# Kernel tuning notes

Hardware: AMD Instinct MI355X
Metric: run time of the kernel (lower is better)

Reference implementation:

```python
import jax, jax.numpy as jnp
import numpy as np

N_HEADS = 16
HEAD_DIM = 64
LN_EPS = 1e-5


def setup_inputs() -> dict:
    key = jax.random.key(0)
    k1, k2, k3 = jax.random.split(key, 3)
    b, n, d = 4, 2048, 1024
    inner = N_HEADS * HEAD_DIM  # 1024
    x = jax.random.normal(k1, (b, n, d), dtype=jnp.float32)
    ln_gamma = jnp.ones((d,), dtype=jnp.float32)
    ln_beta = jnp.zeros((d,), dtype=jnp.float32)
    # torch Linear weights are [out_features, in_features]
    W_qkv = jax.random.normal(k2, (3 * inner, d), dtype=jnp.float32) * (d ** -0.5)
    W_out = jax.random.normal(k3, (d, inner), dtype=jnp.float32) * (inner ** -0.5)
    return {"x": x, "ln_gamma": ln_gamma, "ln_beta": ln_beta,
            "W_qkv": W_qkv, "W_out": W_out}


def reference(x, ln_gamma, ln_beta, W_qkv, W_out):
    b, n, d = x.shape
    scale = HEAD_DIM ** -0.5
    # LayerNorm over last dim
    mu = jnp.mean(x, axis=-1, keepdims=True)
    var = jnp.mean(jnp.square(x - mu), axis=-1, keepdims=True)
    xn = (x - mu) * jax.lax.rsqrt(var + LN_EPS) * ln_gamma + ln_beta
    # QKV projection (Linear, no bias): y = x @ W^T
    qkv = jnp.einsum('bnd,ed->bne', xn, W_qkv)  # [b, n, 3*inner]
    qkv = qkv.reshape(b, n, 3, N_HEADS, HEAD_DIM)
    q, k, v = (jnp.transpose(qkv[:, :, i], (0, 2, 1, 3)) for i in range(3))  # [b,h,n,hd]
    scores = jnp.einsum('bhqd,bhkd->bhqk', q, k) * scale  # [b,h,n,n]
    attn = jax.nn.softmax(scores, axis=-1)
    out = jnp.einsum('bhqk,bhkd->bhqd', attn, v)  # [b,h,n,hd]
    out = jnp.transpose(out, (0, 2, 1, 3)).reshape(b, n, N_HEADS * HEAD_DIM)
    return jnp.einsum('bni,di->bnd', out, W_out)
```

## Files before the change

### kernel.cpp

```cpp
#include <hip/hip_runtime.h>


typedef _Float16 h16;
typedef __attribute__((ext_vector_type(8))) _Float16 h16x8;
typedef __attribute__((ext_vector_type(4))) _Float16 h16x4;
typedef __attribute__((ext_vector_type(2))) _Float16 h16x2;
typedef __attribute__((ext_vector_type(4))) float f32x4;

#define B_ 4
#define S_ 2048
#define D_ 1024

static __device__ __forceinline__ void async16(void* lds, const void* g) {
  __builtin_amdgcn_global_load_lds((const __attribute__((address_space(1))) void*)g,
                                   (__attribute__((address_space(3))) void*)lds,
                                   16, 0, 0);
}

static __device__ __forceinline__ float ex2(float x) {
  float r;
  asm("v_exp_f32 %0, %1" : "=v"(r) : "v"(x));
  return r;
}

static __device__ __forceinline__ h16x2 pk2(float a, float b) {
  h16x2 r;
  asm("v_cvt_pkrtz_f16_f32 %0, %1, %2" : "=v"(r) : "v"(a), "v"(b));
  return r;
}

union U8 { h16x8 v; h16x2 h[4]; };

__global__ __launch_bounds__(256) void prep_k(const float* __restrict__ x,
                                              const float* __restrict__ g,
                                              const float* __restrict__ be,
                                              h16* __restrict__ xn,
                                              const float* __restrict__ wq,
                                              h16* __restrict__ wqkv,
                                              const float* __restrict__ wo,
                                              h16* __restrict__ wout) {
  const int bid = blockIdx.x;
  const int tid = threadIdx.x;
  if (bid < 8192) {
    const int row = bid;
    const float4 v = ((const float4*)(x + (size_t)row * D_))[tid];
    float s = v.x + v.y + v.z + v.w;
    float s2 = v.x * v.x + v.y * v.y + v.z * v.z + v.w * v.w;
#pragma unroll
    for (int msk = 1; msk < 64; msk <<= 1) {
      s += __shfl_xor(s, msk);
      s2 += __shfl_xor(s2, msk);
    }
    __shared__ float red[8];
    const int wv = tid >> 6, ln = tid & 63;
    if (ln == 0) { red[wv] = s; red[wv + 4] = s2; }
    __syncthreads();
    s = red[0] + red[1] + red[2] + red[3];
    s2 = red[4] + red[5] + red[6] + red[7];
    const float mu = s * (1.f / D_);
    const float rs = rsqrtf(s2 * (1.f / D_) - mu * mu + 1e-5f);
    const float4 gv = ((const float4*)g)[tid];
    const float4 bv = ((const float4*)be)[tid];
    h16x4 o;
    o[0] = (h16)((v.x - mu) * rs * gv.x + bv.x);
    o[1] = (h16)((v.y - mu) * rs * gv.y + bv.y);
    o[2] = (h16)((v.z - mu) * rs * gv.z + bv.z);
    o[3] = (h16)((v.w - mu) * rs * gv.w + bv.w);
    *(h16x4*)(xn + (size_t)row * D_ + tid * 4) = o;
  } else if (bid < 8192 + 3072) {
    const int i = (bid - 8192) * 256 + tid;
    const float4 v = ((const float4*)wq)[i];
    h16x4 r;
    r[0] = (h16)v.x; r[1] = (h16)v.y; r[2] = (h16)v.z; r[3] = (h16)v.w;
    *(h16x4*)(wqkv + (size_t)i * 4) = r;
  } else {
    const int i = (bid - 8192 - 3072) * 256 + tid;
    const float4 v = ((const float4*)wo)[i];
    h16x4 r;
    r[0] = (h16)v.x; r[1] = (h16)v.y; r[2] = (h16)v.z; r[3] = (h16)v.w;
    *(h16x4*)(wout + (size_t)i * 4) = r;
  }
}

__global__ __launch_bounds__(256) void vt_k(const h16* __restrict__ qkv,
                                            h16* __restrict__ vT) {
  __shared__ h16 T[64 * 72];
  const int tid = threadIdx.x;
  const int kv0 = blockIdx.x * 64;
  const int bh = blockIdx.y;
  const int b = bh >> 4, h = bh & 15;
#pragma unroll
  for (int it = 0; it < 2; ++it) {
    const int s = tid + it * 256;
    const int kv = s >> 3, sl = s & 7;
    const int wsl = sl ^ ((kv >> 3) & 7);
    const h16x8 v = *(const h16x8*)(qkv + (size_t)(b * S_ + kv0 + kv) * 3072 + 2048 + h * 64 + sl * 8);
    *(h16x8*)(T + kv * 72 + wsl * 8) = v;
  }
  __syncthreads();
#pragma unroll
  for (int it = 0; it < 2; ++it) {
    const int s = tid + it * 256;
    const int d = s >> 3, sl = s & 7;
    h16x8 v;
#pragma unroll
    for (int j = 0; j < 8; ++j) {
      const int kv = sl * 8 + j;
      v[j] = T[kv * 72 + (((d >> 3) ^ sl) & 7) * 8 + (d & 7)];
    }
    *(h16x8*)(vT + (size_t)(bh * 64 + d) * 2048 + kv0 + sl * 8) = v;
  }
}

template <int BN>
__global__ __launch_bounds__(256, 2) void gemm2(const h16* __restrict__ A, int lda,
                                                const h16* __restrict__ Bm,
                                                float* __restrict__ Cf,
                                                h16* __restrict__ Ch,
                                                int M, int N, int K,
                                                int scale_cols, float scale) {
  constexpr int NB = BN / 32;
  constexpr int JF = BN / 32;
  __shared__ __align__(16) h16 As[2][128 * 64];
  __shared__ __align__(16) h16 Bs[2][BN * 64];
  const int tid = threadIdx.x;
  const int wv = tid >> 6, ln = tid & 63;
  const int l15 = ln & 15, l4 = ln >> 4;
  const int row0 = blockIdx.x * 128, col0 = blockIdx.y * BN;
  const int wm = (wv >> 1) * 64, wn = (wv & 1) * (BN / 2);
  f32x4 acc[4][JF] = {};

  const int srow = wv * 8 + (ln >> 3);
  const int sslot = (ln & 7) ^ ((ln >> 3) & 7);
  const h16* ag = A + (size_t)(row0 + srow) * lda + sslot * 8;
  const h16* bg = Bm + (size_t)(col0 + srow) * K + sslot * 8;

  auto stage = [&](int buf, int t) {
    const size_t k_ = (size_t)t * 64;
#pragma unroll
    for (int c = 0; c < 4; ++c)
      async16((char*)As[buf] + c * 4096 + wv * 1024, ag + (size_t)(c * 32) * lda + k_);
#pragma unroll
    for (int c = 0; c < NB; ++c)
      async16((char*)Bs[buf] + c * 4096 + wv * 1024, bg + (size_t)(c * 32) * K + k_);
  };

  auto compute = [&](int buf) {
    const h16* Ab_ = As[buf];
    const h16* Bb_ = Bs[buf];
#pragma unroll
    for (int ks = 0; ks < 2; ++ks) {
      h16x8 af[4], bf[JF];
#pragma unroll
      for (int i = 0; i < 4; ++i)
        af[i] = *(const h16x8*)(Ab_ + (wm + i * 16 + l15) * 64 +
                                (((ks * 4 + l4) ^ (l15 & 7)) * 8));
#pragma unroll
      for (int j = 0; j < JF; ++j)
        bf[j] = *(const h16x8*)(Bb_ + (wn + j * 16 + l15) * 64 +
                                (((ks * 4 + l4) ^ (l15 & 7)) * 8));
      __builtin_amdgcn_s_setprio(1);
#pragma unroll
      for (int i = 0; i < 4; ++i)
#pragma unroll
        for (int j = 0; j < JF; ++j)
          acc[i][j] = __builtin_amdgcn_mfma_f32_16x16x32_f16(af[i], bf[j], acc[i][j], 0, 0, 0);
      __builtin_amdgcn_s_setprio(0);
    }
  };

  stage(0, 0);
  for (int t = 0; t < 16; ++t) {
    asm volatile("s_waitcnt vmcnt(0) lgkmcnt(0)" ::: "memory");
    __builtin_amdgcn_sched_barrier(0);
    __builtin_amdgcn_s_barrier();
    __builtin_amdgcn_sched_barrier(0);
    if (t + 1 < 16) stage((t + 1) & 1, t + 1);
    compute(t & 1);
  }

#pragma unroll
  for (int i = 0; i < 4; ++i)
#pragma unroll
    for (int j = 0; j < JF; ++j) {
      const int col = col0 + wn + j * 16 + l15;
      const float sc = (col < scale_cols) ? scale : 1.f;
#pragma unroll
      for (int r = 0; r < 4; ++r) {
        const int row = row0 + wm + i * 16 + l4 * 4 + r;
        const float vv = acc[i][j][r] * sc;
        if (Ch) Ch[(size_t)row * N + col] = (h16)vv;
        else    Cf[(size_t)row * N + col] = vv;
      }
    }
}

__global__ __launch_bounds__(512) void attn_k(h16* __restrict__ qkv,
                                              const h16* __restrict__ vT) {
  __shared__ __align__(16) h16 Ks[2][2][64 * 64];
  __shared__ __align__(16) h16 Vs[2][2][64 * 64];
  const int tid = threadIdx.x;
  const int wv = tid >> 6, ln = tid & 63;
  const int l15 = ln & 15, l4 = ln >> 4;
  const int bh = blockIdx.x;
  const int b = bh >> 4, h = bh & 15;
  const size_t rb = (size_t)b * S_;
  const int qb = blockIdx.y * 256 + wv * 32;

  h16x8 qf[2][2];
#pragma unroll
  for (int qb2 = 0; qb2 < 2; ++qb2)
#pragma unroll
    for (int ks = 0; ks < 2; ++ks)
      qf[qb2][ks] = *(const h16x8*)(qkv + (rb + qb + qb2 * 16 + l15) * 3072 + h * 64 + ks * 32 + l4 * 8);

  f32x4 o[2][4] = {};
  f32x4 lsum[2] = {};
  h16x8 ones8;
#pragma unroll
  for (int j = 0; j < 8; ++j) ones8[j] = (h16)1.f;

  const int srow = wv * 8 + (ln >> 3);
  const int ssl = (ln & 7) ^ (srow & 7);
  const h16* kgb = qkv + (rb + srow) * 3072 + 1024 + h * 64 + ssl * 8;

  const int vd = tid >> 3;
  const int s8 = tid & 7;
  const int vks = s8 >> 2, vb0b = s8 & 1, vhi = (s8 >> 1) & 1;
  const int vd7 = vd & 7;
  const h16* vgb = vT + (size_t)(bh * 64 + vd) * 2048 + s8 * 8;
  const int dstA = vd * 64 + (((vks * 4 + (vb0b * 2)) ^ vd7) * 8) + vhi * 4;
  const int dstB = vd * 64 + (((vks * 4 + (vb0b * 2 + 1)) ^ vd7) * 8) + vhi * 4;

  int jro[4], slx[2];
#pragma unroll
  for (int j = 0; j < 4; ++j) jro[j] = (j * 16 + l15) * 64;
#pragma unroll
  for (int ks = 0; ks < 2; ++ks) slx[ks] = ((ks * 4 + l4) ^ (l15 & 7)) * 8;

  h16x8 va0, va1, vb0, vb1;

#define ISSUEK2(BUF, P) do {                                                 \
    const h16* kg_ = kgb + (size_t)(2 * (P)) * 64 * 3072;                    \
    async16((char*)Ks[BUF][0] + wv * 1024, kg_);                             \
    async16((char*)Ks[BUF][1] + wv * 1024, kg_ + (size_t)64 * 3072);         \
  } while (0)

#define VLOAD2(P, R0, R1) do {                                               \
    R0 = *(const h16x8*)(vgb + (2 * (P)) * 64);                              \
    R1 = *(const h16x8*)(vgb + (2 * (P) + 1) * 64);                          \
  } while (0)

#define VSTOREM2(BUF, S0, S1) do {                                           \
    *(h16x4*)(Vs[BUF][0] + dstA) = __builtin_shufflevector(S0, S0, 0, 1, 2, 3); \
    *(h16x4*)(Vs[BUF][0] + dstB) = __builtin_shufflevector(S0, S0, 4, 5, 6, 7); \
    *(h16x4*)(Vs[BUF][1] + dstA) = __builtin_shufflevector(S1, S1, 0, 1, 2, 3); \
    *(h16x4*)(Vs[BUF][1] + dstB) = __builtin_shufflevector(S1, S1, 4, 5, 6, 7); \
  } while (0)

#define COMPUTE1(Kb_, Vb_) do {                                              \
    f32x4 st[2][4] = {};                                                     \
    __builtin_amdgcn_s_setprio(1);                                           \
    _Pragma("unroll")                                                        \
    for (int ks = 0; ks < 2; ++ks) {                                         \
      h16x8 kb[4];                                                           \
      _Pragma("unroll")                                                      \
      for (int jb = 0; jb < 4; ++jb)                                         \
        kb[jb] = *(const h16x8*)(Kb_ + jro[jb] + slx[ks]);                   \
      _Pragma("unroll")                                                      \
      for (int qq = 0; qq < 2; ++qq)                                         \
        _Pragma("unroll")                                                    \
        for (int jb = 0; jb < 4; ++jb)                                       \
          st[qq][jb] = __builtin_amdgcn_mfma_f32_16x16x32_f16(kb[jb], qf[qq][ks], st[qq][jb], 0, 0, 0); \
    }                                                                        \
    __builtin_amdgcn_s_setprio(0);                                           \
    h16x8 vfr[2][4];                                                         \
    _Pragma("unroll")                                                        \
    for (int ks = 0; ks < 2; ++ks)                                           \
      _Pragma("unroll")                                                      \
      for (int jd = 0; jd < 4; ++jd)                                         \
        vfr[ks][jd] = *(const h16x8*)(Vb_ + jro[jd] + slx[ks]);              \
    _Pragma("unroll")                                                        \
    for (int qq = 0; qq < 2; ++qq) {                                         \
      h16x8 pa[2];                                                           \
      _Pragma("unroll")                                                      \
      for (int ks = 0; ks < 2; ++ks) {                                       \
        U8 u_;                                                               \
        u_.h[0] = pk2(ex2(st[qq][2 * ks][0]), ex2(st[qq][2 * ks][1]));       \
        u_.h[1] = pk2(ex2(st[qq][2 * ks][2]), ex2(st[qq][2 * ks][3]));       \
        u_.h[2] = pk2(ex2(st[qq][2 * ks + 1][0]), ex2(st[qq][2 * ks + 1][1])); \
        u_.h[3] = pk2(ex2(st[qq][2 * ks + 1][2]), ex2(st[qq][2 * ks + 1][3])); \
        pa[ks] = u_.v;                                                       \
      }                                                                      \
      __builtin_amdgcn_s_setprio(1);                                         \
      _Pragma("unroll")                                                      \
      for (int jd = 0; jd < 4; ++jd)                                         \
        o[qq][jd] = __builtin_amdgcn_mfma_f32_16x16x32_f16(pa[0], vfr[0][jd], o[qq][jd], 0, 0, 0); \
      lsum[qq] = __builtin_amdgcn_mfma_f32_16x16x32_f16(pa[0], ones8, lsum[qq], 0, 0, 0); \
      _Pragma("unroll")                                                      \
      for (int jd = 0; jd < 4; ++jd)                                         \
        o[qq][jd] = __builtin_amdgcn_mfma_f32_16x16x32_f16(pa[1], vfr[1][jd], o[qq][jd], 0, 0, 0); \
      lsum[qq] = __builtin_amdgcn_mfma_f32_16x16x32_f16(pa[1], ones8, lsum[qq], 0, 0, 0); \
      __builtin_amdgcn_s_setprio(0);                                         \
    }                                                                        \
  } while (0)

#define COMPUTE2(BUF) do {                                                   \
    COMPUTE1((Ks[BUF][0]), (Vs[BUF][0]));                                    \
    COMPUTE1((Ks[BUF][1]), (Vs[BUF][1]));                                    \
  } while (0)

#define ENDBAR(VM) do {                                                      \
    asm volatile("s_waitcnt vmcnt(" #VM ") lgkmcnt(0)" ::: "memory");        \
    __builtin_amdgcn_sched_barrier(0);                                       \
    __builtin_amdgcn_s_barrier();                                            \
  } while (0)

#define BODYP(P, VM, VS0, VS1, VL0, VL1) do {                                \
    VSTOREM2(((P) + 1) & 1, VS0, VS1);                                       \
    ISSUEK2(((P) + 1) & 1, (P) + 1);                                         \
    if ((P) + 2 < 16) VLOAD2((P) + 2, VL0, VL1);                             \
    COMPUTE2((P) & 1);                                                       \
    ENDBAR(VM);                                                              \
  } while (0)

  ISSUEK2(0, 0);
  VLOAD2(0, va0, va1);
  VSTOREM2(0, va0, va1);
  VLOAD2(1, vb0, vb1);
  ENDBAR(2);

  for (int p = 0; p < 14; p += 2) {
    BODYP(p + 0, 2, vb0, vb1, va0, va1);
    BODYP(p + 1, 2, va0, va1, vb0, vb1);
  }
  BODYP(14, 0, vb0, vb1, va0, va1);
  COMPUTE2(1);

#pragma unroll
  for (int qb2 = 0; qb2 < 2; ++qb2) {
    f32x4 iv;
#pragma unroll
    for (int r = 0; r < 4; ++r) iv[r] = 1.f / lsum[qb2][r];
#pragma unroll
    for (int jd = 0; jd < 4; ++jd)
#pragma unroll
      for (int r = 0; r < 4; ++r) {
        const size_t row = rb + qb + qb2 * 16 + l4 * 4 + r;
        qkv[row * 3072 + h * 64 + jd * 16 + l15] = (h16)(o[qb2][jd][r] * iv[r]);
      }
  }
#undef ISSUEK2
#undef VLOAD2
#undef VSTOREM2
#undef COMPUTE1
#undef COMPUTE2
#undef ENDBAR
#undef BODYP
}

extern "C" void kernel_launch(void* const* d_in, const int* in_sizes, int n_in,
                              void* d_out, int out_size, void* d_ws, size_t ws_size,
                              hipStream_t stream) {
  const float* x  = (const float*)d_in[0];
  const float* g  = (const float*)d_in[1];
  const float* be = (const float*)d_in[2];
  const float* wq = (const float*)d_in[3];
  const float* wo = (const float*)d_in[4];
  float* out = (float*)d_out;

  char* ws = (char*)d_ws;
  h16* xn   = (h16*)ws;
  h16* wqkv = (h16*)(ws + 16777216);
  h16* wout = (h16*)(ws + 23068672);
  h16* qkv  = (h16*)(ws + 25165824);
  h16* vT   = xn;

  prep_k<<<dim3(8192 + 3072 + 1024), dim3(256), 0, stream>>>(x, g, be, xn, wq, wqkv, wo, wout);
  gemm2<192><<<dim3(64, 16), dim3(256), 0, stream>>>(xn, 1024, wqkv, (float*)nullptr, qkv,
                                                     8192, 3072, 1024, 1024, 0.18033688f);
  vt_k<<<dim3(32, 64), dim3(256), 0, stream>>>(qkv, vT);
  attn_k<<<dim3(64, 8), dim3(512), 0, stream>>>(qkv, vT);
  gemm2<128><<<dim3(64, 8), dim3(256), 0, stream>>>(qkv, 3072, wout, out, (h16*)nullptr,
                                                    8192, 1024, 1024, 0, 1.f);
}
```

Before: 174.2 us.

## Replace GEMM with 8-wave 256x128 tile kernel using triple-buffered interleaved loads

New measurement: 191.3 us. 9.8% more time.

```diff
diff --git a/kernel.cpp b/kernel.cpp
--- a/kernel.cpp
+++ b/kernel.cpp
@@ -112,87 +112,124 @@
   }
 }
 
-template <int BN>
-__global__ __launch_bounds__(256, 2) void gemm2(const h16* __restrict__ A, int lda,
-                                                const h16* __restrict__ Bm,
-                                                float* __restrict__ Cf,
-                                                h16* __restrict__ Ch,
-                                                int M, int N, int K,
-                                                int scale_cols, float scale) {
-  constexpr int NB = BN / 32;
-  constexpr int JF = BN / 32;
-  __shared__ __align__(16) h16 As[2][128 * 64];
-  __shared__ __align__(16) h16 Bs[2][BN * 64];
+__global__ __launch_bounds__(512) void gemm8(const h16* __restrict__ A, int lda,
+                                             const h16* __restrict__ Bm,
+                                             float* __restrict__ Cf,
+                                             h16* __restrict__ Ch,
+                                             int M, int N, int K,
+                                             int scale_cols, float scale) {
+  __shared__ __align__(16) h16 As[3][256 * 64];
+  __shared__ __align__(16) h16 Bs[3][128 * 64];
   const int tid = threadIdx.x;
   const int wv = tid >> 6, ln = tid & 63;
   const int l15 = ln & 15, l4 = ln >> 4;
-  const int row0 = blockIdx.x * 128, col0 = blockIdx.y * BN;
-  const int wm = (wv >> 1) * 64, wn = (wv & 1) * (BN / 2);
-  f32x4 acc[4][JF] = {};
+  const int row0 = blockIdx.x * 256, col0 = blockIdx.y * 128;
+  const int wr = (wv >> 2) * 128, wc = (wv & 3) * 32;
+  f32x4 acc[8][2] = {};
 
   const int srow = wv * 8 + (ln >> 3);
   const int sslot = (ln & 7) ^ ((ln >> 3) & 7);
   const h16* ag = A + (size_t)(row0 + srow) * lda + sslot * 8;
   const h16* bg = Bm + (size_t)(col0 + srow) * K + sslot * 8;
 
-  auto stage = [&](int buf, int t) {
-    const size_t k_ = (size_t)t * 64;
-#pragma unroll
-    for (int c = 0; c < 4; ++c)
-      async16((char*)As[buf] + c * 4096 + wv * 1024, ag + (size_t)(c * 32) * lda + k_);
-#pragma unroll
-    for (int c = 0; c < NB; ++c)
-      async16((char*)Bs[buf] + c * 4096 + wv * 1024, bg + (size_t)(c * 32) * K + k_);
-  };
-
-  auto compute = [&](int buf) {
-    const h16* Ab_ = As[buf];
-    const h16* Bb_ = Bs[buf];
-#pragma unroll
-    for (int ks = 0; ks < 2; ++ks) {
-      h16x8 af[4], bf[JF];
-#pragma unroll
-      for (int i = 0; i < 4; ++i)
-        af[i] = *(const h16x8*)(Ab_ + (wm + i * 16 + l15) * 64 +
-                                (((ks * 4 + l4) ^ (l15 & 7)) * 8));
-#pragma unroll
-      for (int j = 0; j < JF; ++j)
-        bf[j] = *(const h16x8*)(Bb_ + (wn + j * 16 + l15) * 64 +
-                                (((ks * 4 + l4) ^ (l15 & 7)) * 8));
-      __builtin_amdgcn_s_setprio(1);
-#pragma unroll
-      for (int i = 0; i < 4; ++i)
-#pragma unroll
-        for (int j = 0; j < JF; ++j)
-          acc[i][j] = __builtin_amdgcn_mfma_f32_16x16x32_f16(af[i], bf[j], acc[i][j], 0, 0, 0);
-      __builtin_amdgcn_s_setprio(0);
-    }
-  };
-
-  stage(0, 0);
-  for (int t = 0; t < 16; ++t) {
-    asm volatile("s_waitcnt vmcnt(0) lgkmcnt(0)" ::: "memory");
-    __builtin_amdgcn_sched_barrier(0);
-    __builtin_amdgcn_s_barrier();
-    __builtin_amdgcn_sched_barrier(0);
-    if (t + 1 < 16) stage((t + 1) & 1, t + 1);
-    compute(t & 1);
-  }
-
-#pragma unroll
-  for (int i = 0; i < 4; ++i)
-#pragma unroll
-    for (int j = 0; j < JF; ++j) {
-      const int col = col0 + wn + j * 16 + l15;
+#define GLA(BUF, T) do {                                                     \
+    const size_t k_ = (size_t)(T) * 64;                                      \
+    async16((char*)As[BUF] + wv * 1024,          ag + k_);                   \
+    async16((char*)As[BUF] + 8192 + wv * 1024,   ag + (size_t)64 * lda + k_);\
+    async16((char*)As[BUF] + 16384 + wv * 1024,  ag + (size_t)128 * lda + k_);\
+    async16((char*)As[BUF] + 24576 + wv * 1024,  ag + (size_t)192 * lda + k_);\
+  } while (0)
+
+#define GLB(BUF, T) do {                                                     \
+    const size_t k_ = (size_t)(T) * 64;                                      \
+    async16((char*)Bs[BUF] + wv * 1024,          bg + k_);                   \
+    async16((char*)Bs[BUF] + 8192 + wv * 1024,   bg + (size_t)64 * K + k_);  \
+  } while (0)
+
+#define RDFRAGS(BUF, KS, AF, BF) do {                                        \
+    const h16* Ab_ = As[BUF];                                                \
+    const h16* Bb_ = Bs[BUF];                                                \
+    _Pragma("unroll")                                                        \
+    for (int i = 0; i < 8; ++i)                                              \
+      AF[i] = *(const h16x8*)(Ab_ + (wr + i * 16 + l15) * 64 +               \
+                              ((((KS) * 4 + l4) ^ (l15 & 7)) * 8));          \
+    _Pragma("unroll")                                                        \
+    for (int j = 0; j < 2; ++j)                                              \
+      BF[j] = *(const h16x8*)(Bb_ + (wc + j * 16 + l15) * 64 +               \
+                              ((((KS) * 4 + l4) ^ (l15 & 7)) * 8));          \
+  } while (0)
+
+#define MFMAS(AF, BF) do {                                                   \
+    __builtin_amdgcn_s_setprio(1);                                           \
+    _Pragma("unroll")                                                        \
+    for (int i = 0; i < 8; ++i)                                              \
+      _Pragma("unroll")                                                      \
+      for (int j = 0; j < 2; ++j)                                            \
+        acc[i][j] = __builtin_amdgcn_mfma_f32_16x16x32_f16(AF[i], BF[j], acc[i][j], 0, 0, 0); \
+    __builtin_amdgcn_s_setprio(0);                                           \
+  } while (0)
+
+#define SB() __builtin_amdgcn_sched_barrier(0)
+#define BAR() do { SB(); __builtin_amdgcn_s_barrier(); SB(); } while (0)
+
+#define GBODY(T, BUF, VM) do {                                               \
+    {                                                                        \
+      h16x8 af[8], bf[2];                                                    \
+      RDFRAGS(BUF, 0, af, bf);                                               \
+      if ((T) + 2 < 16) GLA(((BUF) + 2) % 3, (T) + 2);                       \
+      BAR();                                                                 \
+      asm volatile("s_waitcnt lgkmcnt(0)" ::: "memory"); SB();               \
+      MFMAS(af, bf);                                                         \
+      BAR();                                                                 \
+    }                                                                        \
+    {                                                                        \
+      h16x8 af[8], bf[2];                                                    \
+      RDFRAGS(BUF, 1, af, bf);                                               \
+      if ((T) + 2 < 16) GLB(((BUF) + 2) % 3, (T) + 2);                       \
+      asm volatile("s_waitcnt vmcnt(" #VM ")" ::: "memory"); SB();           \
+      BAR();                                                                 \
+      asm volatile("s_waitcnt lgkmcnt(0)" ::: "memory"); SB();               \
+      MFMAS(af, bf);                                                         \
+      BAR();                                                                 \
+    }                                                                        \
+  } while (0)
+
+  GLA(0, 0); GLB(0, 0);
+  GLA(1, 1); GLB(1, 1);
+  asm volatile("s_waitcnt vmcnt(6)" ::: "memory"); SB();
+  BAR();
+
+  for (int t3 = 0; t3 < 12; t3 += 3) {
+    GBODY(t3 + 0, 0, 6);
+    GBODY(t3 + 1, 1, 6);
+    GBODY(t3 + 2, 2, 6);
+  }
+  GBODY(12, 0, 6);
+  GBODY(13, 1, 6);
+  GBODY(14, 2, 0);
+  GBODY(15, 0, 0);
+
+#pragma unroll
+  for (int i = 0; i < 8; ++i)
+#pragma unroll
+    for (int j = 0; j < 2; ++j) {
+      const int col = col0 + wc + j * 16 + l15;
       const float sc = (col < scale_cols) ? scale : 1.f;
 #pragma unroll
       for (int r = 0; r < 4; ++r) {
-        const int row = row0 + wm + i * 16 + l4 * 4 + r;
+        const int row = row0 + wr + i * 16 + l4 * 4 + r;
         const float vv = acc[i][j][r] * sc;
         if (Ch) Ch[(size_t)row * N + col] = (h16)vv;
         else    Cf[(size_t)row * N + col] = vv;
       }
     }
+#undef GLA
+#undef GLB
+#undef RDFRAGS
+#undef MFMAS
+#undef SB
+#undef BAR
+#undef GBODY
 }
 
 __global__ __launch_bounds__(512) void attn_k(h16* __restrict__ qkv,
@@ -377,10 +414,10 @@
   h16* vT   = xn;
 
   prep_k<<<dim3(8192 + 3072 + 1024), dim3(256), 0, stream>>>(x, g, be, xn, wq, wqkv, wo, wout);
-  gemm2<192><<<dim3(64, 16), dim3(256), 0, stream>>>(xn, 1024, wqkv, (float*)nullptr, qkv,
-                                                     8192, 3072, 1024, 1024, 0.18033688f);
+  gemm8<<<dim3(32, 24), dim3(512), 0, stream>>>(xn, 1024, wqkv, (float*)nullptr, qkv,
+                                                8192, 3072, 1024, 1024, 0.18033688f);
   vt_k<<<dim3(32, 64), dim3(256), 0, stream>>>(qkv, vT);
   attn_k<<<dim3(64, 8), dim3(512), 0, stream>>>(qkv, vT);
-  gemm2<128><<<dim3(64, 8), dim3(256), 0, stream>>>(qkv, 3072, wout, out, (h16*)nullptr,
-                                                    8192, 1024, 1024, 0, 1.f);
-}
+  gemm8<<<dim3(32, 8), dim3(512), 0, stream>>>(qkv, 3072, wout, out, (h16*)nullptr,
+                                               8192, 1024, 1024, 0, 1.f);
+}
```
